# Performance work log

Hardware: AMD Instinct MI355X
Metric: run time of the kernel (lower is better)

Reference implementation:

```python
import jax, jax.numpy as jnp
import numpy as np

N = 100000
E = 1600000
G = 64  # number of graphs
H = 128
BN_EPS = 1e-5


def setup_inputs() -> dict:
    key = jax.random.key(0)
    ks = jax.random.split(key, 12)
    x = jax.random.normal(ks[0], (N, 3), dtype=jnp.float32)
    edge_index = jax.random.randint(ks[1], (2, E), 0, N, dtype=jnp.int64)
    batch = jnp.sort(jax.random.randint(ks[2], (N,), 0, G, dtype=jnp.int64))
    W1 = jax.random.normal(ks[3], (3, H), dtype=jnp.float32) * 0.3
    W2 = jax.random.normal(ks[4], (H, H), dtype=jnp.float32) * 0.05
    W3 = jax.random.normal(ks[5], (H, H), dtype=jnp.float32) * 0.05
    lin_W = jax.random.normal(ks[6], (H, 2), dtype=jnp.float32) * 0.05
    d = {
        'x': x, 'edge_index': edge_index, 'batch': batch,
        'W1': W1, 'b1': jnp.zeros((H,), jnp.float32),
        'W2': W2, 'b2': jnp.zeros((H,), jnp.float32),
        'W3': W3, 'b3': jnp.zeros((H,), jnp.float32),
        'lin_W': lin_W, 'lin_b': jnp.zeros((2,), jnp.float32),
    }
    for i, kk in zip((1, 2, 3), ks[7:10]):
        d[f'bn{i}_g'] = jnp.ones((H,), jnp.float32)
        d[f'bn{i}_b'] = jnp.zeros((H,), jnp.float32)
        d[f'bn{i}_m'] = jnp.zeros((H,), jnp.float32)
        d[f'bn{i}_v'] = jax.random.uniform(kk, (H,), dtype=jnp.float32, minval=0.5, maxval=1.5)
    return d


def _gcn(x, src, dst, norm, W, b):
    # GCNConv: out = scatter_add(norm * (xW)[src], dst) + b
    h = x @ W
    msg = h[src] * norm[:, None]
    agg = jax.ops.segment_sum(msg, dst, num_segments=N)
    return agg + b


def _bn_eval(x, g, b, m, v):
    return (x - m) * jax.lax.rsqrt(v + BN_EPS) * g + b


def reference(x, edge_index, batch, W1, b1, W2, b2, W3, b3,
              bn1_g, bn1_b, bn1_m, bn1_v,
              bn2_g, bn2_b, bn2_m, bn2_v,
              bn3_g, bn3_b, bn3_m, bn3_v,
              lin_W, lin_b):
    loop = jnp.arange(N, dtype=edge_index.dtype)
    src = jnp.concatenate([edge_index[0], loop])
    dst = jnp.concatenate([edge_index[1], loop])
    # symmetric normalization with self-loops: deg from destination nodes
    deg = jax.ops.segment_sum(jnp.ones_like(dst, dtype=x.dtype), dst, num_segments=N)
    dinv = jnp.where(deg > 0, jax.lax.rsqrt(deg), 0.0)
    norm = dinv[src] * dinv[dst]

    h = jax.nn.relu(_bn_eval(_gcn(x, src, dst, norm, W1, b1), bn1_g, bn1_b, bn1_m, bn1_v))
    h = jax.nn.relu(_bn_eval(_gcn(h, src, dst, norm, W2, b2), bn2_g, bn2_b, bn2_m, bn2_v))
    h = jax.nn.relu(_bn_eval(_gcn(h, src, dst, norm, W3, b3), bn3_g, bn3_b, bn3_m, bn3_v))
    # dropout is identity in eval mode
    sums = jax.ops.segment_sum(h, batch, num_segments=G)
    cnts = jax.ops.segment_sum(jnp.ones((N,), h.dtype), batch, num_segments=G)
    pooled = sums / jnp.maximum(cnts, 1.0)[:, None]
    return pooled @ lin_W + lin_b
```

## Files before the change

### kernel.cpp

```cpp
#include <hip/hip_runtime.h>

#define NN 100000
#define EE 1600000
#define GG 64
#define HH 128
#define BN_EPS 1e-5f

#define CB 782
#define NB 256
#define TILE 6250

typedef unsigned short ushort_t;
typedef __attribute__((ext_vector_type(8))) short bf16x8;
typedef __attribute__((ext_vector_type(4))) float f32x4;

#define MFMA16 __builtin_amdgcn_mfma_f32_16x16x32_bf16

#define WFRAG_LO 16384

static __device__ inline ushort_t f2bf(float f) {
    unsigned u = __float_as_uint(f);
    unsigned r = (u + 0x7FFF + ((u >> 16) & 1)) >> 16;
    return (ushort_t)r;
}
static __device__ inline float bf2f(ushort_t b) {
    return __uint_as_float(((unsigned)b) << 16);
}
#define BFLO(u) __uint_as_float(((unsigned)(u)) << 16)
#define BFHI(u) __uint_as_float(((unsigned)(u)) & 0xFFFF0000u)


__global__ __launch_bounds__(256) void k_hist(const int* __restrict__ ei,
                                              int* __restrict__ histG) {
    __shared__ int h[CB];
    int t = threadIdx.x;
    for (int i = t; i < CB; i += 256) h[i] = 0;
    __syncthreads();
    int e0 = blockIdx.x * TILE;
    for (int i = t; i < TILE; i += 256) {
        int d = ei[EE + e0 + i];
        atomicAdd(&h[d >> 7], 1);
    }
    __syncthreads();
    for (int i = t; i < CB; i += 256) histG[blockIdx.x * CB + i] = h[i];
}

__global__ __launch_bounds__(NB) void k_bscan(int* __restrict__ histG,
                                              int* __restrict__ total) {
    __shared__ int sh[NB];
    int t = threadIdx.x;
    int c = blockIdx.x;
    sh[t] = histG[t * CB + c];
    __syncthreads();
    for (int d = 1; d < NB; d <<= 1) {
        int x = (t >= d) ? sh[t - d] : 0;
        __syncthreads();
        sh[t] += x;
        __syncthreads();
    }
    histG[t * CB + c] = (t > 0) ? sh[t - 1] : 0;
    if (t == NB - 1) total[c] = sh[NB - 1];
}

__global__ __launch_bounds__(1024) void k_cbase(const int* __restrict__ total,
                                                int* __restrict__ cbase) {
    __shared__ int sh[1024];
    int t = threadIdx.x;
    sh[t] = (t < CB) ? total[t] : 0;
    __syncthreads();
    for (int d = 1; d < 1024; d <<= 1) {
        int x = (t >= d) ? sh[t - d] : 0;
        __syncthreads();
        sh[t] += x;
        __syncthreads();
    }
    if (t < CB) cbase[t] = (t > 0) ? sh[t - 1] : 0;
    if (t == CB - 1) cbase[CB] = sh[t];
}

__global__ __launch_bounds__(256) void k_cscatter(const int* __restrict__ ei,
                                                  const int* __restrict__ histG,
                                                  const int* __restrict__ cbase,
                                                  int* __restrict__ metaS) {
    __shared__ int base_l[CB];
    __shared__ int cur_l[CB];
    int t = threadIdx.x;
    int b = blockIdx.x;
    for (int i = t; i < CB; i += 256) {
        base_l[i] = cbase[i] + histG[b * CB + i];
        cur_l[i] = 0;
    }
    __syncthreads();
    int e0 = b * TILE;
    for (int i = t; i < TILE; i += 256) {
        int s = ei[e0 + i];
        int d = ei[EE + e0 + i];
        int c = d >> 7;
        int p = base_l[c] + atomicAdd(&cur_l[c], 1);
        metaS[p] = s | ((d & 127) << 17);
    }
}

__global__ __launch_bounds__(256) void k_fine(const int* __restrict__ metaS,
                                              const int* __restrict__ cbase,
                                              int* __restrict__ cnt,
                                              int* __restrict__ offs,
                                              int* __restrict__ col,
                                              float* __restrict__ dinv) {
    __shared__ int hist[128];
    __shared__ int scn[128];
    __shared__ int cur[128];
    int t = threadIdx.x;
    int c = blockIdx.x;
    int lo = cbase[c], hi = cbase[c + 1];
    if (t < 128) hist[t] = 0;
    __syncthreads();
    for (int r = lo + t; r < hi; r += 256) atomicAdd(&hist[metaS[r] >> 17], 1);
    __syncthreads();
    if (t < 128) scn[t] = hist[t];
    __syncthreads();
    for (int d = 1; d < 128; d <<= 1) {
        int x = (t >= d && t < 128) ? scn[t - d] : 0;
        __syncthreads();
        if (t < 128) scn[t] += x;
        __syncthreads();
    }
    if (t < 128) {
        int excl = (t > 0) ? scn[t - 1] : 0;
        cur[t] = excl;
        int node = c * 128 + t;
        if (node < NN) {
            cnt[node] = hist[t];
            offs[node] = lo + excl;
            dinv[node] = rsqrtf((float)(hist[t] + 1));
        }
    }
    __syncthreads();
    for (int r = lo + t; r < hi; r += 256) {
        int pk = metaS[r];
        int s = pk & 0x1FFFF;
        int idx = atomicAdd(&cur[pk >> 17], 1);
        col[lo + idx] = s;
    }
}


__global__ __launch_bounds__(64) void k_gcnt(const int* __restrict__ batch,
                                             int* __restrict__ gcnt) {
    int g = threadIdx.x;
    int lo = 0, hi = NN;
    while (lo < hi) { int mid = (lo + hi) >> 1; if (batch[mid] < g) lo = mid + 1; else hi = mid; }
    int a = lo;
    lo = 0; hi = NN;
    int g1 = g + 1;
    while (lo < hi) { int mid = (lo + hi) >> 1; if (batch[mid] < g1) lo = mid + 1; else hi = mid; }
    gcnt[g] = lo - a;
}


__global__ __launch_bounds__(256) void k_wprep(const float* __restrict__ W2,
                                               const float* __restrict__ W3,
                                               ushort_t* __restrict__ w2f,
                                               ushort_t* __restrict__ w3f) {
    const float* W = (blockIdx.x & 8) ? W3 : W2;
    ushort_t* o = (blockIdx.x & 8) ? w3f : w2f;
    int tid = ((int)blockIdx.x & 7) * 256 + threadIdx.x;
    int l = tid & 63;
    int kb = ((tid >> 6) & 3) * 32 + (l >> 4) * 8;
    int n = (tid >> 8) * 16 + (l & 15);
    unsigned hp[4], lp[4];
#pragma unroll
    for (int p = 0; p < 4; p++) {
        float v0 = W[(size_t)(kb + 2 * p) * HH + n];
        float v1 = W[(size_t)(kb + 2 * p + 1) * HH + n];
        ushort_t h0 = f2bf(v0), h1 = f2bf(v1);
        ushort_t l0 = f2bf(v0 - bf2f(h0)), l1 = f2bf(v1 - bf2f(h1));
        hp[p] = (unsigned)h0 | ((unsigned)h1 << 16);
        lp[p] = (unsigned)l0 | ((unsigned)l1 << 16);
    }
    *(uint4*)&o[(size_t)tid * 8] = make_uint4(hp[0], hp[1], hp[2], hp[3]);
    *(uint4*)&o[WFRAG_LO + (size_t)tid * 8] = make_uint4(lp[0], lp[1], lp[2], lp[3]);
}


__global__ __launch_bounds__(256) void k_aggx(const float* __restrict__ x,
                                              const int* __restrict__ offs,
                                              const int* __restrict__ cnt,
                                              const int* __restrict__ col,
                                              const float* __restrict__ dinv,
                                              float4* __restrict__ agg) {
    int tid = threadIdx.x;
    int wave = tid >> 6;
    int lane = tid & 63;
    int grp = lane >> 4;
    int l = lane & 15;
    int n = blockIdx.x * 16 + wave * 4 + grp;
    float dv = dinv[n];
    int base = offs[n], cn = cnt[n];
    float a0 = 0.f, a1 = 0.f, a2 = 0.f;
    for (int i = l; i < cn; i += 16) {
        int s = col[base + i];
        float w = dinv[s] * dv;
        a0 += w * x[s * 3 + 0];
        a1 += w * x[s * 3 + 1];
        a2 += w * x[s * 3 + 2];
    }
#pragma unroll
    for (int off = 8; off >= 1; off >>= 1) {
        a0 += __shfl_xor(a0, off, 16);
        a1 += __shfl_xor(a1, off, 16);
        a2 += __shfl_xor(a2, off, 16);
    }
    if (l == 0) {
        float w0 = dv * dv;
        a0 += w0 * x[n * 3 + 0];
        a1 += w0 * x[n * 3 + 1];
        a2 += w0 * x[n * 3 + 2];
        agg[n] = make_float4(a0, a1, a2, 0.f);
    }
}


__global__ __launch_bounds__(256) void k_mml1(const float4* __restrict__ agg,
                                              const float* __restrict__ W1,
                                              const float* __restrict__ b1,
                                              const float* __restrict__ g1,
                                              const float* __restrict__ bb1,
                                              const float* __restrict__ m1,
                                              const float* __restrict__ v1,
                                              const ushort_t* __restrict__ Wf,
                                              ushort_t* __restrict__ outB) {
    __shared__ float4 ag[64];
    __shared__ __align__(16) ushort_t xh[2][64 * HH];
    int tid = threadIdx.x;
    int row0 = blockIdx.x * 64;
    if (tid < 64) {
        int gr = row0 + tid;
        ag[tid] = (gr < NN) ? agg[gr] : make_float4(0.f, 0.f, 0.f, 0.f);
    }
    __syncthreads();
    {
        int c = tid & 127;
        int rh = tid >> 7;
        float w0 = W1[c], w1 = W1[128 + c], w2 = W1[256 + c];
        float sc = g1[c] * rsqrtf(v1[c] + BN_EPS);
        float sh = (b1[c] - m1[c]) * sc + bb1[c];
#pragma unroll
        for (int i = 0; i < 32; i++) {
            int r = 2 * i + rh;
            float4 a = ag[r];
            float t = fmaxf((a.x * w0 + a.y * w1 + a.z * w2) * sc + sh, 0.f);
            ushort_t hi = f2bf(t);
            ushort_t lo = f2bf(t - bf2f(hi));
            int idx = r * HH + (c ^ ((r & 7) << 3));
            xh[0][idx] = hi;
            xh[1][idx] = lo;
        }
    }
    __syncthreads();

    int w = tid >> 6, l = tid & 63;
    int r_lo = l & 15, kgrp = l >> 4;
    int row_l = w * 16 + r_lo;
    f32x4 acc[8];
#pragma unroll
    for (int nt = 0; nt < 8; nt++) acc[nt] = (f32x4){0.f, 0.f, 0.f, 0.f};

#pragma unroll
    for (int kk = 0; kk < 4; kk++) {
        int ke = kk * 32 + kgrp * 8;
        int idx = row_l * HH + (ke ^ ((row_l & 7) << 3));
        bf16x8 ahf = *(const bf16x8*)&xh[0][idx];
        bf16x8 alf = *(const bf16x8*)&xh[1][idx];
#pragma unroll
        for (int nt = 0; nt < 8; nt++) {
            int fo = ((((nt << 2) | kk) << 6) + l) * 8;
            bf16x8 bh = *(const bf16x8*)&Wf[fo];
            bf16x8 bl = *(const bf16x8*)&Wf[WFRAG_LO + fo];
            acc[nt] = MFMA16(ahf, bh, acc[nt], 0, 0, 0);
            acc[nt] = MFMA16(ahf, bl, acc[nt], 0, 0, 0);
            acc[nt] = MFMA16(alf, bh, acc[nt], 0, 0, 0);
        }
    }
#pragma unroll
    for (int q = 0; q < 4; q++) {
        int gr = row0 + w * 16 + kgrp * 4 + q;
        if (gr < NN) {
            size_t rb = (size_t)gr * HH + r_lo;
#pragma unroll
            for (int nt = 0; nt < 8; nt++)
                outB[rb + nt * 16] = f2bf(acc[nt][q]);
        }
    }
}


__global__ __launch_bounds__(256) void k_mm(const ushort_t* __restrict__ xin,
                                            const ushort_t* __restrict__ Wf,
                                            ushort_t* __restrict__ outB) {
    int tid = threadIdx.x;
    int w = tid >> 6, l = tid & 63;
    int row0 = blockIdx.x * 128 + w * 32;
    int r_lo = l & 15, kgrp = l >> 4;
    f32x4 acc[2][8];
#pragma unroll
    for (int rt = 0; rt < 2; rt++)
#pragma unroll
        for (int nt = 0; nt < 8; nt++) acc[rt][nt] = (f32x4){0.f, 0.f, 0.f, 0.f};

    bf16x8 za = {0, 0, 0, 0, 0, 0, 0, 0};
#pragma unroll
    for (int kk = 0; kk < 4; kk++) {
        int ke = kk * 32 + kgrp * 8;
        int ra0 = row0 + r_lo;
        int ra1 = row0 + 16 + r_lo;
        bf16x8 a0 = (ra0 < NN) ? *(const bf16x8*)&xin[(size_t)ra0 * HH + ke] : za;
        bf16x8 a1 = (ra1 < NN) ? *(const bf16x8*)&xin[(size_t)ra1 * HH + ke] : za;
#pragma unroll
        for (int nt = 0; nt < 8; nt++) {
            int fo = ((((nt << 2) | kk) << 6) + l) * 8;
            bf16x8 bh = *(const bf16x8*)&Wf[fo];
            bf16x8 bl = *(const bf16x8*)&Wf[WFRAG_LO + fo];
            acc[0][nt] = MFMA16(a0, bh, acc[0][nt], 0, 0, 0);
            acc[0][nt] = MFMA16(a0, bl, acc[0][nt], 0, 0, 0);
            acc[1][nt] = MFMA16(a1, bh, acc[1][nt], 0, 0, 0);
            acc[1][nt] = MFMA16(a1, bl, acc[1][nt], 0, 0, 0);
        }
    }
#pragma unroll
    for (int rt = 0; rt < 2; rt++)
#pragma unroll
        for (int q = 0; q < 4; q++) {
            int gr = row0 + rt * 16 + kgrp * 4 + q;
            if (gr < NN) {
                size_t rb = (size_t)gr * HH + r_lo;
#pragma unroll
                for (int nt = 0; nt < 8; nt++)
                    outB[rb + nt * 16] = f2bf(acc[rt][nt][q]);
            }
        }
}


template<int POOL>
__global__ __launch_bounds__(256) void k_agg(const ushort_t* __restrict__ t,
                                             const int* __restrict__ offs,
                                             const int* __restrict__ cnt,
                                             const int* __restrict__ col,
                                             const float* __restrict__ dinv,
                                             const int* __restrict__ batch,
                                             const float* __restrict__ bias,
                                             const float* __restrict__ g,
                                             const float* __restrict__ bb,
                                             const float* __restrict__ m,
                                             const float* __restrict__ v,
                                             ushort_t* __restrict__ out,
                                             float* __restrict__ gsum) {
    int l = threadIdx.x & 63;
    int nw = gridDim.x << 2;
    int wid = ((int)blockIdx.x << 2) + (threadIdx.x >> 6);
    int grp = l >> 4, sub = l & 15;
    int c0 = sub << 3;
    float sc[8], sh[8];
#pragma unroll
    for (int e = 0; e < 8; e++) {
        int c = c0 + e;
        float s_ = g[c] * rsqrtf(v[c] + BN_EPS);
        sc[e] = s_;
        sh[e] = (bias[c] - m[c]) * s_ + bb[c];
    }
    int chunk = (NN + nw - 1) / nw;
    int d0 = wid * chunk;
    int d1 = min(NN, d0 + chunk);
    float pacc[8];
    int curg = -1;
    if (POOL) {
#pragma unroll
        for (int e = 0; e < 8; e++) pacc[e] = 0.f;
        if (d0 < d1) curg = batch[d0];
    }
    for (int d = d0; d < d1; d++) {
        float dv = dinv[d];
        int base = offs[d], cn = cnt[d];
        float acc[8];
        if (grp == 0) {
            float w0 = dv * dv;
            const int4 pk = *(const int4*)&t[(size_t)d * HH + c0];
            acc[0] = w0 * BFLO(pk.x); acc[1] = w0 * BFHI(pk.x);
            acc[2] = w0 * BFLO(pk.y); acc[3] = w0 * BFHI(pk.y);
            acc[4] = w0 * BFLO(pk.z); acc[5] = w0 * BFHI(pk.z);
            acc[6] = w0 * BFLO(pk.w); acc[7] = w0 * BFHI(pk.w);
        } else {
#pragma unroll
            for (int e = 0; e < 8; e++) acc[e] = 0.f;
        }
        for (int cb = 0; cb < cn; cb += 64) {
            int ce = min(64, cn - cb);
            int sv = 0;
            float wv = 0.f;
            if (l < ce) {
                sv = col[base + cb + l];
                wv = dinv[sv] * dv;
            }
            int cf = ce & ~3;
#pragma unroll 4
            for (int e0 = 0; e0 < cf; e0 += 4) {
                int ss = __shfl(sv, e0 + grp, 64);
                float ww = __shfl(wv, e0 + grp, 64);
                const int4 pk = *(const int4*)&t[(size_t)ss * HH + c0];
                acc[0] += ww * BFLO(pk.x); acc[1] += ww * BFHI(pk.x);
                acc[2] += ww * BFLO(pk.y); acc[3] += ww * BFHI(pk.y);
                acc[4] += ww * BFLO(pk.z); acc[5] += ww * BFHI(pk.z);
                acc[6] += ww * BFLO(pk.w); acc[7] += ww * BFHI(pk.w);
            }
            if (cf < ce) {
                int idx = cf + grp;
                int ss = __shfl(sv, idx, 64);
                float ww = __shfl(wv, idx, 64);
                if (idx < ce) {
                    const int4 pk = *(const int4*)&t[(size_t)ss * HH + c0];
                    acc[0] += ww * BFLO(pk.x); acc[1] += ww * BFHI(pk.x);
                    acc[2] += ww * BFLO(pk.y); acc[3] += ww * BFHI(pk.y);
                    acc[4] += ww * BFLO(pk.z); acc[5] += ww * BFHI(pk.z);
                    acc[6] += ww * BFLO(pk.w); acc[7] += ww * BFHI(pk.w);
                }
            }
        }
#pragma unroll
        for (int e = 0; e < 8; e++) {
            acc[e] += __shfl_xor(acc[e], 16, 64);
            acc[e] += __shfl_xor(acc[e], 32, 64);
        }
        if (POOL) {
            int gnow = batch[d];
            if (gnow != curg) {
                if (l < 16) {
#pragma unroll
                    for (int e = 0; e < 8; e++)
                        atomicAdd(&gsum[curg * HH + c0 + e], pacc[e]);
                }
#pragma unroll
                for (int e = 0; e < 8; e++) pacc[e] = 0.f;
                curg = gnow;
            }
#pragma unroll
            for (int e = 0; e < 8; e++)
                pacc[e] += fmaxf(acc[e] * sc[e] + sh[e], 0.f);
        } else {
            if (l < 16) {
                float r0 = fmaxf(acc[0] * sc[0] + sh[0], 0.f);
                float r1 = fmaxf(acc[1] * sc[1] + sh[1], 0.f);
                float r2 = fmaxf(acc[2] * sc[2] + sh[2], 0.f);
                float r3 = fmaxf(acc[3] * sc[3] + sh[3], 0.f);
                float r4 = fmaxf(acc[4] * sc[4] + sh[4], 0.f);
                float r5 = fmaxf(acc[5] * sc[5] + sh[5], 0.f);
                float r6 = fmaxf(acc[6] * sc[6] + sh[6], 0.f);
                float r7 = fmaxf(acc[7] * sc[7] + sh[7], 0.f);
                int4 o;
                o.x = (int)f2bf(r0) | ((int)f2bf(r1) << 16);
                o.y = (int)f2bf(r2) | ((int)f2bf(r3) << 16);
                o.z = (int)f2bf(r4) | ((int)f2bf(r5) << 16);
                o.w = (int)f2bf(r6) | ((int)f2bf(r7) << 16);
                *(int4*)&out[(size_t)d * HH + c0] = o;
            }
        }
    }
    if (POOL && curg >= 0 && l < 16) {
#pragma unroll
        for (int e = 0; e < 8; e++)
            atomicAdd(&gsum[curg * HH + c0 + e], pacc[e]);
    }
}


__global__ void k_head(const float* __restrict__ gsum, const int* __restrict__ gcnt,
                       const float* __restrict__ linW, const float* __restrict__ linb,
                       float* __restrict__ out) {
    int t = threadIdx.x;
    int gr = t >> 1, j = t & 1;
    float inv = 1.0f / fmaxf((float)gcnt[gr], 1.0f);
    float acc = 0.f;
    for (int c = 0; c < HH; c++) acc += gsum[gr * HH + c] * linW[c * 2 + j];
    out[t] = acc * inv + linb[j];
}


static inline size_t al256(size_t x) { return (x + 255) & ~(size_t)255; }

extern "C" void kernel_launch(void* const* d_in, const int* in_sizes, int n_in,
                              void* d_out, int out_size, void* d_ws, size_t ws_size,
                              hipStream_t stream) {
    const float* x    = (const float*)d_in[0];
    const int*   ei   = (const int*)d_in[1];
    const int*   batch= (const int*)d_in[2];
    const float* W1   = (const float*)d_in[3];
    const float* b1   = (const float*)d_in[4];
    const float* W2   = (const float*)d_in[5];
    const float* b2   = (const float*)d_in[6];
    const float* W3   = (const float*)d_in[7];
    const float* b3   = (const float*)d_in[8];
    const float* linW = (const float*)d_in[9];
    const float* linb = (const float*)d_in[10];
    const float* bn1g = (const float*)d_in[11];
    const float* bn1b = (const float*)d_in[12];
    const float* bn1m = (const float*)d_in[13];
    const float* bn1v = (const float*)d_in[14];
    const float* bn2g = (const float*)d_in[15];
    const float* bn2b = (const float*)d_in[16];
    const float* bn2m = (const float*)d_in[17];
    const float* bn2v = (const float*)d_in[18];
    const float* bn3g = (const float*)d_in[19];
    const float* bn3b = (const float*)d_in[20];
    const float* bn3m = (const float*)d_in[21];
    const float* bn3v = (const float*)d_in[22];
    float* out = (float*)d_out;

    char* ws = (char*)d_ws;
    size_t off = 0;
    int*    histG  = (int*)(ws + off);    off += al256((size_t)NB * CB * 4);
    int*    total  = (int*)(ws + off);    off += al256((size_t)CB * 4);
    int*    cbase  = (int*)(ws + off);    off += al256((size_t)(CB + 1) * 4);
    int*    cnt    = (int*)(ws + off);    off += al256((size_t)NN * 4);
    int*    offs   = (int*)(ws + off);    off += al256((size_t)NN * 4);
    float*  dinv   = (float*)(ws + off);  off += al256((size_t)NN * 4);
    int*    col    = (int*)(ws + off);    off += al256((size_t)EE * 4);
    ushort_t* w2f  = (ushort_t*)(ws + off); off += al256((size_t)2 * WFRAG_LO * 2);
    ushort_t* w3f  = (ushort_t*)(ws + off); off += al256((size_t)2 * WFRAG_LO * 2);
    float4* agg    = (float4*)(ws + off); off += al256((size_t)NN * 16);
    char*   bufA   = (char*)(ws + off);   off += al256((size_t)NN * HH * 2);
    char*   bufB   = (char*)(ws + off);   off += al256((size_t)NN * HH * 4);
    float*  gsum   = (float*)(ws + off);  off += (size_t)GG * HH * 4;
    int*    gcnt   = (int*)(ws + off);    off += al256((size_t)GG * 4);

    int* metaS = (int*)bufB;
    ushort_t* tB = (ushort_t*)bufB;
    ushort_t* hB = (ushort_t*)bufA;

    hipMemsetAsync(gsum, 0, (size_t)GG * HH * 4, stream);

    k_wprep<<<16, 256, 0, stream>>>(W2, W3, w2f, w3f);
    k_gcnt<<<1, 64, 0, stream>>>(batch, gcnt);

    k_hist<<<NB, 256, 0, stream>>>(ei, histG);
    k_bscan<<<CB, NB, 0, stream>>>(histG, total);
    k_cbase<<<1, 1024, 0, stream>>>(total, cbase);
    k_cscatter<<<NB, 256, 0, stream>>>(ei, histG, cbase, metaS);
    k_fine<<<CB, 256, 0, stream>>>(metaS, cbase, cnt, offs, col, dinv);

    k_aggx<<<NN / 16, 256, 0, stream>>>(x, offs, cnt, col, dinv, agg);

    k_mml1<<<(NN + 63) / 64, 256, 0, stream>>>(agg, W1, b1, bn1g, bn1b, bn1m, bn1v,
                                               w2f, tB);
    k_agg<0><<<2048, 256, 0, stream>>>(tB, offs, cnt, col, dinv, batch,
                                       b2, bn2g, bn2b, bn2m, bn2v, hB, nullptr);

    k_mm<<<(NN + 127) / 128, 256, 0, stream>>>(hB, w3f, tB);
    k_agg<1><<<2048, 256, 0, stream>>>(tB, offs, cnt, col, dinv, batch,
                                       b3, bn3g, bn3b, bn3m, bn3v, nullptr, gsum);

    k_head<<<1, 128, 0, stream>>>(gsum, gcnt, linW, linb, out);
}
```

Measured before the change: 452.2 us.

## Restructure GCN aggregation to half-wave per node with 4-channel lanes

Result: slower. 462.6 us (+2.3%).

```diff
diff --git a/kernel.cpp b/kernel.cpp
--- a/kernel.cpp
+++ b/kernel.cpp
@@ -26,8 +26,6 @@
 static __device__ inline float bf2f(ushort_t b) {
     return __uint_as_float(((unsigned)b) << 16);
 }
-#define BFLO(u) __uint_as_float(((unsigned)(u)) << 16)
-#define BFHI(u) __uint_as_float(((unsigned)(u)) & 0xFFFF0000u)
 
 
 __global__ __launch_bounds__(256) void k_hist(const int* __restrict__ ei,
@@ -356,119 +354,97 @@
                                              const float* __restrict__ v,
                                              ushort_t* __restrict__ out,
                                              float* __restrict__ gsum) {
-    int l = threadIdx.x & 63;
-    int nw = gridDim.x << 2;
-    int wid = ((int)blockIdx.x << 2) + (threadIdx.x >> 6);
-    int grp = l >> 4, sub = l & 15;
-    int c0 = sub << 3;
-    float sc[8], sh[8];
-#pragma unroll
-    for (int e = 0; e < 8; e++) {
-        int c = c0 + e;
-        float s_ = g[c] * rsqrtf(v[c] + BN_EPS);
-        sc[e] = s_;
-        sh[e] = (bias[c] - m[c]) * s_ + bb[c];
-    }
-    int chunk = (NN + nw - 1) / nw;
-    int d0 = wid * chunk;
-    int d1 = min(NN, d0 + chunk);
-    float pacc[8];
+    int wave = threadIdx.x >> 6;
+    int lane = threadIdx.x & 63;
+    int half = lane >> 5;
+    int l = lane & 31;
+    int c0 = l * 4;
+
+    float4 gg = *(const float4*)&g[c0];
+    float4 vv = *(const float4*)&v[c0];
+    float4 mm = *(const float4*)&m[c0];
+    float4 bv = *(const float4*)&bb[c0];
+    float4 bi = *(const float4*)&bias[c0];
+    float sc0 = gg.x * rsqrtf(vv.x + BN_EPS);
+    float sc1 = gg.y * rsqrtf(vv.y + BN_EPS);
+    float sc2 = gg.z * rsqrtf(vv.z + BN_EPS);
+    float sc3 = gg.w * rsqrtf(vv.w + BN_EPS);
+    float sh0 = (bi.x - mm.x) * sc0 + bv.x;
+    float sh1 = (bi.y - mm.y) * sc1 + bv.y;
+    float sh2 = (bi.z - mm.z) * sc2 + bv.z;
+    float sh3 = (bi.w - mm.w) * sc3 + bv.w;
+
+    int d0, d1;
+    float p0 = 0.f, p1 = 0.f, p2 = 0.f, p3 = 0.f;
     int curg = -1;
     if (POOL) {
-#pragma unroll
-        for (int e = 0; e < 8; e++) pacc[e] = 0.f;
-        if (d0 < d1) curg = batch[d0];
-    }
+        int hw = blockIdx.x * 8 + wave * 2 + half;
+        d0 = hw * 5;
+        d1 = d0 + 5;
+        curg = batch[d0];
+    } else {
+        d0 = blockIdx.x * 8 + wave * 2 + half;
+        d1 = d0 + 1;
+    }
+
     for (int d = d0; d < d1; d++) {
         float dv = dinv[d];
+        float w0 = dv * dv;
+        ushort4 selfR = *(const ushort4*)&t[(size_t)d * HH + c0];
+        float a0 = bf2f(selfR.x) * w0;
+        float a1 = bf2f(selfR.y) * w0;
+        float a2 = bf2f(selfR.z) * w0;
+        float a3 = bf2f(selfR.w) * w0;
         int base = offs[d], cn = cnt[d];
-        float acc[8];
-        if (grp == 0) {
-            float w0 = dv * dv;
-            const int4 pk = *(const int4*)&t[(size_t)d * HH + c0];
-            acc[0] = w0 * BFLO(pk.x); acc[1] = w0 * BFHI(pk.x);
-            acc[2] = w0 * BFLO(pk.y); acc[3] = w0 * BFHI(pk.y);
-            acc[4] = w0 * BFLO(pk.z); acc[5] = w0 * BFHI(pk.z);
-            acc[6] = w0 * BFLO(pk.w); acc[7] = w0 * BFHI(pk.w);
-        } else {
-#pragma unroll
-            for (int e = 0; e < 8; e++) acc[e] = 0.f;
-        }
-        for (int cb = 0; cb < cn; cb += 64) {
-            int ce = min(64, cn - cb);
-            int sv = 0;
-            float wv = 0.f;
-            if (l < ce) {
-                sv = col[base + cb + l];
-                wv = dinv[sv] * dv;
+        for (int ib = 0; ib < cn; ib += 32) {
+            int i = ib + l;
+            int s = 0;
+            float w = 0.f;
+            if (i < cn) {
+                s = col[base + i];
+                w = dinv[s] * dv;
             }
-            int cf = ce & ~3;
-#pragma unroll 4
-            for (int e0 = 0; e0 < cf; e0 += 4) {
-                int ss = __shfl(sv, e0 + grp, 64);
-                float ww = __shfl(wv, e0 + grp, 64);
-                const int4 pk = *(const int4*)&t[(size_t)ss * HH + c0];
-                acc[0] += ww * BFLO(pk.x); acc[1] += ww * BFHI(pk.x);
-                acc[2] += ww * BFLO(pk.y); acc[3] += ww * BFHI(pk.y);
-                acc[4] += ww * BFLO(pk.z); acc[5] += ww * BFHI(pk.z);
-                acc[6] += ww * BFLO(pk.w); acc[7] += ww * BFHI(pk.w);
+            int lim = min(32, cn - ib);
+#pragma unroll 8
+            for (int j = 0; j < lim; j++) {
+                int ss = __shfl(s, j, 32);
+                float ww = __shfl(w, j, 32);
+                ushort4 tv = *(const ushort4*)&t[(size_t)ss * HH + c0];
+                a0 += ww * bf2f(tv.x);
+                a1 += ww * bf2f(tv.y);
+                a2 += ww * bf2f(tv.z);
+                a3 += ww * bf2f(tv.w);
             }
-            if (cf < ce) {
-                int idx = cf + grp;
-                int ss = __shfl(sv, idx, 64);
-                float ww = __shfl(wv, idx, 64);
-                if (idx < ce) {
-                    const int4 pk = *(const int4*)&t[(size_t)ss * HH + c0];
-                    acc[0] += ww * BFLO(pk.x); acc[1] += ww * BFHI(pk.x);
-                    acc[2] += ww * BFLO(pk.y); acc[3] += ww * BFHI(pk.y);
-                    acc[4] += ww * BFLO(pk.z); acc[5] += ww * BFHI(pk.z);
-                    acc[6] += ww * BFLO(pk.w); acc[7] += ww * BFHI(pk.w);
-                }
-            }
-        }
-#pragma unroll
-        for (int e = 0; e < 8; e++) {
-            acc[e] += __shfl_xor(acc[e], 16, 64);
-            acc[e] += __shfl_xor(acc[e], 32, 64);
-        }
+        }
+        float r0 = fmaxf(a0 * sc0 + sh0, 0.f);
+        float r1 = fmaxf(a1 * sc1 + sh1, 0.f);
+        float r2 = fmaxf(a2 * sc2 + sh2, 0.f);
+        float r3 = fmaxf(a3 * sc3 + sh3, 0.f);
         if (POOL) {
             int gnow = batch[d];
             if (gnow != curg) {
-                if (l < 16) {
-#pragma unroll
-                    for (int e = 0; e < 8; e++)
-                        atomicAdd(&gsum[curg * HH + c0 + e], pacc[e]);
-                }
-#pragma unroll
-                for (int e = 0; e < 8; e++) pacc[e] = 0.f;
+                atomicAdd(&gsum[curg * HH + c0 + 0], p0);
+                atomicAdd(&gsum[curg * HH + c0 + 1], p1);
+                atomicAdd(&gsum[curg * HH + c0 + 2], p2);
+                atomicAdd(&gsum[curg * HH + c0 + 3], p3);
+                p0 = p1 = p2 = p3 = 0.f;
                 curg = gnow;
             }
-#pragma unroll
-            for (int e = 0; e < 8; e++)
-                pacc[e] += fmaxf(acc[e] * sc[e] + sh[e], 0.f);
+            p0 += r0; p1 += r1; p2 += r2; p3 += r3;
         } else {
-            if (l < 16) {
-                float r0 = fmaxf(acc[0] * sc[0] + sh[0], 0.f);
-                float r1 = fmaxf(acc[1] * sc[1] + sh[1], 0.f);
-                float r2 = fmaxf(acc[2] * sc[2] + sh[2], 0.f);
-                float r3 = fmaxf(acc[3] * sc[3] + sh[3], 0.f);
-                float r4 = fmaxf(acc[4] * sc[4] + sh[4], 0.f);
-                float r5 = fmaxf(acc[5] * sc[5] + sh[5], 0.f);
-                float r6 = fmaxf(acc[6] * sc[6] + sh[6], 0.f);
-                float r7 = fmaxf(acc[7] * sc[7] + sh[7], 0.f);
-                int4 o;
-                o.x = (int)f2bf(r0) | ((int)f2bf(r1) << 16);
-                o.y = (int)f2bf(r2) | ((int)f2bf(r3) << 16);
-                o.z = (int)f2bf(r4) | ((int)f2bf(r5) << 16);
-                o.w = (int)f2bf(r6) | ((int)f2bf(r7) << 16);
-                *(int4*)&out[(size_t)d * HH + c0] = o;
-            }
-        }
-    }
-    if (POOL && curg >= 0 && l < 16) {
-#pragma unroll
-        for (int e = 0; e < 8; e++)
-            atomicAdd(&gsum[curg * HH + c0 + e], pacc[e]);
+            ushort4 o;
+            o.x = f2bf(r0);
+            o.y = f2bf(r1);
+            o.z = f2bf(r2);
+            o.w = f2bf(r3);
+            *(ushort4*)&out[(size_t)d * HH + c0] = o;
+        }
+    }
+    if (POOL) {
+        atomicAdd(&gsum[curg * HH + c0 + 0], p0);
+        atomicAdd(&gsum[curg * HH + c0 + 1], p1);
+        atomicAdd(&gsum[curg * HH + c0 + 2], p2);
+        atomicAdd(&gsum[curg * HH + c0 + 3], p3);
     }
 }
 
@@ -551,11 +527,11 @@
 
     k_mml1<<<(NN + 63) / 64, 256, 0, stream>>>(agg, W1, b1, bn1g, bn1b, bn1m, bn1v,
                                                w2f, tB);
-    k_agg<0><<<2048, 256, 0, stream>>>(tB, offs, cnt, col, dinv, batch,
-                                       b2, bn2g, bn2b, bn2m, bn2v, hB, nullptr);
+    k_agg<0><<<NN / 8, 256, 0, stream>>>(tB, offs, cnt, col, dinv, batch,
+                                         b2, bn2g, bn2b, bn2m, bn2v, hB, nullptr);
 
     k_mm<<<(NN + 127) / 128, 256, 0, stream>>>(hB, w3f, tB);
-    k_agg<1><<<2048, 256, 0, stream>>>(tB, offs, cnt, col, dinv, batch,
+    k_agg<1><<<2500, 256, 0, stream>>>(tB, offs, cnt, col, dinv, batch,
                                        b3, bn3g, bn3b, bn3m, bn3v, nullptr, gsum);
 
     k_head<<<1, 128, 0, stream>>>(gsum, gcnt, linW, linb, out);
```
